# Kernel optimization log

Hardware: AMD Instinct MI355X
Metric: run time of the kernel (lower is better)

The kernel has to match this reference:

```python
import jax, jax.numpy as jnp
import numpy as np

NUM_USERS = 500000
NUM_ITEMS = 500000
EMB_DIM = 64
BATCH = 16384
BN_EPS = 1e-5


def setup_inputs() -> dict:
    key = jax.random.key(0)
    ks = jax.random.split(key, 16)
    d = {}
    d["user_ids"] = jax.random.randint(ks[0], (BATCH,), 0, NUM_USERS)
    d["item_ids"] = jax.random.randint(ks[1], (BATCH,), 0, NUM_ITEMS)
    # wide layer: Linear(num_users+num_items, 1) -> weight stored as a flat vector + scalar bias
    d["wide_w"] = jax.random.normal(ks[2], (NUM_USERS + NUM_ITEMS,), jnp.float32) * 0.002
    d["wide_b"] = jnp.zeros((), jnp.float32)
    # embedding tables (init normal std=0.1 as in _init_weights)
    d["user_table"] = jax.random.normal(ks[3], (NUM_USERS, EMB_DIM), jnp.float32) * 0.1
    d["item_table"] = jax.random.normal(ks[4], (NUM_ITEMS, EMB_DIM), jnp.float32) * 0.1
    # deep MLP: 128 -> 256 -> 128 -> 64 -> 1, xavier-ish init, zero bias
    dims = [2 * EMB_DIM, 256, 128, 64]
    for i, (din, dout) in enumerate(zip(dims[:-1], dims[1:]), start=1):
        scale = float(np.sqrt(6.0 / (din + dout)))
        d[f"w{i}"] = jax.random.uniform(ks[4 + i], (din, dout), jnp.float32, -scale, scale)
        d[f"b{i}"] = jnp.zeros((dout,), jnp.float32)
        d[f"g{i}"] = jnp.ones((dout,), jnp.float32)   # BN gamma
        d[f"be{i}"] = jnp.zeros((dout,), jnp.float32)  # BN beta
    scale = float(np.sqrt(6.0 / (64 + 1)))
    d["w4"] = jax.random.uniform(ks[9], (64, 1), jnp.float32, -scale, scale)
    d["b4"] = jnp.zeros((1,), jnp.float32)
    return d


def _bn_eval(h, g, be):
    # eval-mode BatchNorm1d with running_mean=0, running_var=1
    return g * (h * (1.0 / jnp.sqrt(1.0 + BN_EPS))) + be


def reference(user_ids, item_ids, wide_w, wide_b, user_table, item_table,
              w1, b1, g1, be1, w2, b2, g2, be2, w3, b3, g3, be3, w4, b4):
    # Wide path: one_hot(user) @ W.T + one_hot(item) @ W.T + b  ==  gather + sum + bias
    wide = wide_w[user_ids] + wide_w[NUM_USERS + item_ids] + wide_b  # [B]
    # Deep path
    x = jnp.concatenate([user_table[user_ids], item_table[item_ids]], axis=1)  # [B, 128]
    for w, b, g, be in ((w1, b1, g1, be1), (w2, b2, g2, be2), (w3, b3, g3, be3)):
        x = _bn_eval(jax.nn.relu(x @ w + b), g, be)  # Linear -> ReLU -> BN (Dropout=id in eval)
    deep = (x @ w4 + b4)[:, 0]  # [B]
    return wide + deep
```

## Files before the change

### kernel.cpp

```cpp
#include <hip/hip_runtime.h>


#define NT 512
#define TS 32

constexpr int NUM_USERS = 500000;
constexpr float BN_INV = 0.9999950000374997f;

struct __align__(16) Smem {
    float xs[TS * 128];
    float h1[TS * 256];
};

#define FMA4(xk, wv, a)                      \
    do {                                     \
        (a).x = fmaf((xk), (wv).x, (a).x);   \
        (a).y = fmaf((xk), (wv).y, (a).y);   \
        (a).z = fmaf((xk), (wv).z, (a).z);   \
        (a).w = fmaf((xk), (wv).w, (a).w);   \
    } while (0)

template <int K, int N>
__device__ __forceinline__ void mlp_layer(
    const float* __restrict__ w, const float* __restrict__ bias,
    const float* __restrict__ gamma, const float* __restrict__ beta,
    const float* in_lds, float* out_lds, int t)
{
    constexpr int JG = N / 4;
    constexpr int S  = N / 64;
    constexpr int NW = N / 4;

    const int j0 = (t % JG) * 4;
    const int s0 = (t / JG) * S;

    float4 acc[S];
#pragma unroll
    for (int s = 0; s < S; ++s) acc[s] = make_float4(0.f, 0.f, 0.f, 0.f);

    const float4* wp = (const float4*)w + (j0 >> 2);

#pragma unroll 4
    for (int k4 = 0; k4 < K; k4 += 4) {
        float4 wv0 = wp[(k4 + 0) * NW];
        float4 wv1 = wp[(k4 + 1) * NW];
        float4 wv2 = wp[(k4 + 2) * NW];
        float4 wv3 = wp[(k4 + 3) * NW];
        float4 xv[S];
#pragma unroll
        for (int s = 0; s < S; ++s)
            xv[s] = *(const float4*)&in_lds[(s0 + s) * K + k4];
#pragma unroll
        for (int s = 0; s < S; ++s) {
            FMA4(xv[s].x, wv0, acc[s]);
            FMA4(xv[s].y, wv1, acc[s]);
            FMA4(xv[s].z, wv2, acc[s]);
            FMA4(xv[s].w, wv3, acc[s]);
        }
    }

    const float4 bv = *(const float4*)&bias[j0];
    const float4 gv = *(const float4*)&gamma[j0];
    const float4 ev = *(const float4*)&beta[j0];
#pragma unroll
    for (int s = 0; s < S; ++s) {
        float4 o;
        o.x = fmaxf(acc[s].x + bv.x, 0.f) * (gv.x * BN_INV) + ev.x;
        o.y = fmaxf(acc[s].y + bv.y, 0.f) * (gv.y * BN_INV) + ev.y;
        o.z = fmaxf(acc[s].z + bv.z, 0.f) * (gv.z * BN_INV) + ev.z;
        o.w = fmaxf(acc[s].w + bv.w, 0.f) * (gv.w * BN_INV) + ev.w;
        *(float4*)&out_lds[(s0 + s) * N + j0] = o;
    }
}

__global__ __launch_bounds__(NT, 4) void wd_kernel(
    const int* __restrict__ user_ids, const int* __restrict__ item_ids,
    const float* __restrict__ wide_w, const float* __restrict__ wide_b,
    const float* __restrict__ user_table, const float* __restrict__ item_table,
    const float* __restrict__ w1, const float* __restrict__ b1,
    const float* __restrict__ g1, const float* __restrict__ be1,
    const float* __restrict__ w2, const float* __restrict__ b2,
    const float* __restrict__ g2, const float* __restrict__ be2,
    const float* __restrict__ w3, const float* __restrict__ b3,
    const float* __restrict__ g3, const float* __restrict__ be3,
    const float* __restrict__ w4, const float* __restrict__ b4,
    float* __restrict__ out)
{
    __shared__ Smem sm;
    const int t = threadIdx.x;
    const int sbase = blockIdx.x * TS;

    {
        const int s = t >> 4;
        const int p = t & 15;
        const int uid = user_ids[sbase + s];
        const int iid = item_ids[sbase + s];
        ((float4*)&sm.xs[s * 128])[p] =
            ((const float4*)(user_table + (long)uid * 64))[p];
        ((float4*)&sm.xs[s * 128])[16 + p] =
            ((const float4*)(item_table + (long)iid * 64))[p];
    }

    float widev = 0.0f;
    if (t < TS * 8 && (t & 7) == 0) {
        const int s = t >> 3;
        const int uid = user_ids[sbase + s];
        const int iid = item_ids[sbase + s];
        widev = wide_w[uid] + wide_w[NUM_USERS + iid] + wide_b[0];
    }
    __syncthreads();

    mlp_layer<128, 256>(w1, b1, g1, be1, sm.xs, sm.h1, t);
    __syncthreads();
    mlp_layer<256, 128>(w2, b2, g2, be2, sm.h1, sm.xs, t);
    __syncthreads();
    mlp_layer<128, 64 >(w3, b3, g3, be3, sm.xs, sm.h1, t);
    __syncthreads();

    if (t < TS * 8) {
        const int s = t >> 3;
        const int g = t & 7;
        const float* h = &sm.h1[s * 64 + g * 8];
        const float4 ha = *(const float4*)(h);
        const float4 hb = *(const float4*)(h + 4);
        const float4 wa = *(const float4*)(w4 + g * 8);
        const float4 wb = *(const float4*)(w4 + g * 8 + 4);
        float p = ha.x * wa.x + ha.y * wa.y + ha.z * wa.z + ha.w * wa.w
                + hb.x * wb.x + hb.y * wb.y + hb.z * wb.z + hb.w * wb.w;
        p += __shfl_down(p, 4);
        p += __shfl_down(p, 2);
        p += __shfl_down(p, 1);
        if (g == 0) out[sbase + s] = widev + p + b4[0];
    }
}

extern "C" void kernel_launch(void* const* d_in, const int* in_sizes, int n_in,
                              void* d_out, int out_size, void* d_ws, size_t ws_size,
                              hipStream_t stream) {
    (void)in_sizes; (void)n_in; (void)d_ws; (void)ws_size;
    const int*   user_ids   = (const int*)d_in[0];
    const int*   item_ids   = (const int*)d_in[1];
    const float* wide_w     = (const float*)d_in[2];
    const float* wide_b     = (const float*)d_in[3];
    const float* user_table = (const float*)d_in[4];
    const float* item_table = (const float*)d_in[5];
    const float* w1 = (const float*)d_in[6];
    const float* b1 = (const float*)d_in[7];
    const float* g1 = (const float*)d_in[8];
    const float* be1 = (const float*)d_in[9];
    const float* w2 = (const float*)d_in[10];
    const float* b2 = (const float*)d_in[11];
    const float* g2 = (const float*)d_in[12];
    const float* be2 = (const float*)d_in[13];
    const float* w3 = (const float*)d_in[14];
    const float* b3 = (const float*)d_in[15];
    const float* g3 = (const float*)d_in[16];
    const float* be3 = (const float*)d_in[17];
    const float* w4 = (const float*)d_in[18];
    const float* b4 = (const float*)d_in[19];
    float* out = (float*)d_out;

    const int grid = 16384 / TS;
    wd_kernel<<<grid, NT, 0, stream>>>(
        user_ids, item_ids, wide_w, wide_b, user_table, item_table,
        w1, b1, g1, be1, w2, b2, g2, be2, w3, b3, g3, be3, w4, b4, out);
}
```

Baseline: 314.3 us.

## Pad LDS rows and remap waves to feature slices and sample groups

Pads the shared-memory activation rows by four floats so per-sample float4 reads land in different LDS banks. The thread-to-work mapping changes so each wave owns a feature slice and a group of samples, with lanes split across features and samples. The goal is fewer LDS bank conflicts and a wave-level mix of shared weight and activation loads. The cost is more LDS per block, which could lower occupancy, and a different global weight-load coalescing pattern.

Measured after the change: 310.9 us. About the same (-1.1%).

```diff
diff --git a/kernel.cpp b/kernel.cpp
--- a/kernel.cpp
+++ b/kernel.cpp
@@ -8,8 +8,8 @@
 constexpr float BN_INV = 0.9999950000374997f;
 
 struct __align__(16) Smem {
-    float xs[TS * 128];
-    float h1[TS * 256];
+    float xs[TS * 132];
+    float h1[TS * 260];
 };
 
 #define FMA4(xk, wv, a)                      \
@@ -20,37 +20,44 @@
         (a).w = fmaf((xk), (wv).w, (a).w);   \
     } while (0)
 
-template <int K, int N>
+template <int K, int KS, int N, int NS, int FS>
 __device__ __forceinline__ void mlp_layer(
     const float* __restrict__ w, const float* __restrict__ bias,
     const float* __restrict__ gamma, const float* __restrict__ beta,
     const float* in_lds, float* out_lds, int t)
 {
-    constexpr int JG = N / 4;
-    constexpr int S  = N / 64;
-    constexpr int NW = N / 4;
+    constexpr int JG     = FS / 4;
+    constexpr int SG     = 64 / JG;
+    constexpr int NSLICE = N / FS;
+    constexpr int SM     = TS * NSLICE / 8;
+    constexpr int SPL    = SM / SG;
+    constexpr int NW4    = N / 4;
+    static_assert(SPL * SG == SM, "layout");
 
-    const int j0 = (t % JG) * 4;
-    const int s0 = (t / JG) * S;
+    const int wave = t >> 6, lane = t & 63;
+    const int wslice = wave % NSLICE, wsamp = wave / NSLICE;
+    const int jg = lane % JG, sg = lane / JG;
+    const int j0 = wslice * FS + jg * 4;
+    const int s0 = wsamp * SM + sg * SPL;
 
-    float4 acc[S];
+    float4 acc[SPL];
 #pragma unroll
-    for (int s = 0; s < S; ++s) acc[s] = make_float4(0.f, 0.f, 0.f, 0.f);
+    for (int s = 0; s < SPL; ++s) acc[s] = make_float4(0.f, 0.f, 0.f, 0.f);
 
     const float4* wp = (const float4*)w + (j0 >> 2);
 
 #pragma unroll 4
     for (int k4 = 0; k4 < K; k4 += 4) {
-        float4 wv0 = wp[(k4 + 0) * NW];
-        float4 wv1 = wp[(k4 + 1) * NW];
-        float4 wv2 = wp[(k4 + 2) * NW];
-        float4 wv3 = wp[(k4 + 3) * NW];
-        float4 xv[S];
+        float4 wv0 = wp[(k4 + 0) * NW4];
+        float4 wv1 = wp[(k4 + 1) * NW4];
+        float4 wv2 = wp[(k4 + 2) * NW4];
+        float4 wv3 = wp[(k4 + 3) * NW4];
+        float4 xv[SPL];
 #pragma unroll
-        for (int s = 0; s < S; ++s)
-            xv[s] = *(const float4*)&in_lds[(s0 + s) * K + k4];
+        for (int s = 0; s < SPL; ++s)
+            xv[s] = *(const float4*)&in_lds[(s0 + s) * KS + k4];
 #pragma unroll
-        for (int s = 0; s < S; ++s) {
+        for (int s = 0; s < SPL; ++s) {
             FMA4(xv[s].x, wv0, acc[s]);
             FMA4(xv[s].y, wv1, acc[s]);
             FMA4(xv[s].z, wv2, acc[s]);
@@ -62,13 +69,13 @@
     const float4 gv = *(const float4*)&gamma[j0];
     const float4 ev = *(const float4*)&beta[j0];
 #pragma unroll
-    for (int s = 0; s < S; ++s) {
+    for (int s = 0; s < SPL; ++s) {
         float4 o;
         o.x = fmaxf(acc[s].x + bv.x, 0.f) * (gv.x * BN_INV) + ev.x;
         o.y = fmaxf(acc[s].y + bv.y, 0.f) * (gv.y * BN_INV) + ev.y;
         o.z = fmaxf(acc[s].z + bv.z, 0.f) * (gv.z * BN_INV) + ev.z;
         o.w = fmaxf(acc[s].w + bv.w, 0.f) * (gv.w * BN_INV) + ev.w;
-        *(float4*)&out_lds[(s0 + s) * N + j0] = o;
+        *(float4*)&out_lds[(s0 + s) * NS + j0] = o;
     }
 }
 
@@ -94,10 +101,9 @@
         const int p = t & 15;
         const int uid = user_ids[sbase + s];
         const int iid = item_ids[sbase + s];
-        ((float4*)&sm.xs[s * 128])[p] =
-            ((const float4*)(user_table + (long)uid * 64))[p];
-        ((float4*)&sm.xs[s * 128])[16 + p] =
-            ((const float4*)(item_table + (long)iid * 64))[p];
+        float4* row = (float4*)&sm.xs[s * 132];
+        row[p]      = ((const float4*)(user_table + (long)uid * 64))[p];
+        row[16 + p] = ((const float4*)(item_table + (long)iid * 64))[p];
     }
 
     float widev = 0.0f;
@@ -109,17 +115,17 @@
     }
     __syncthreads();
 
-    mlp_layer<128, 256>(w1, b1, g1, be1, sm.xs, sm.h1, t);
+    mlp_layer<128, 132, 256, 260, 64>(w1, b1, g1, be1, sm.xs, sm.h1, t);
     __syncthreads();
-    mlp_layer<256, 128>(w2, b2, g2, be2, sm.h1, sm.xs, t);
+    mlp_layer<256, 260, 128, 132, 32>(w2, b2, g2, be2, sm.h1, sm.xs, t);
     __syncthreads();
-    mlp_layer<128, 64 >(w3, b3, g3, be3, sm.xs, sm.h1, t);
+    mlp_layer<128, 132,  64,  68, 32>(w3, b3, g3, be3, sm.xs, sm.h1, t);
     __syncthreads();
 
     if (t < TS * 8) {
         const int s = t >> 3;
         const int g = t & 7;
-        const float* h = &sm.h1[s * 64 + g * 8];
+        const float* h = &sm.h1[s * 68 + g * 8];
         const float4 ha = *(const float4*)(h);
         const float4 hb = *(const float4*)(h + 4);
         const float4 wa = *(const float4*)(w4 + g * 8);
```
